# Kernel optimization log

Measured on AMD Instinct MI355X. Metric: run time of the kernel, lower is better.

The kernel has to match this reference:

```python
import jax, jax.numpy as jnp
import numpy as np

N_NODES = 50000
N_EDGES = 800000
N_RELS = 16
D = 128


def _rgcn_layer(h, W, b, loop_w, gate_w, src, dst, rel, norm, apply_relu, n_nodes):
    # Transform all node features by every relation weight once: [R, N, D_out].
    # Equivalent to DGL bmm_maybe_select's per-edge W[rel] bmm, but avoids an
    # [E, D, D] gather of weights.
    h_all = jnp.einsum('nd,rde->rne', h, W)
    msg = h_all[rel, src]                                    # [E, D_out]
    msg = msg * norm                                         # edge norm scaling
    gate_logit = jnp.einsum('nd,rd->rn', h, gate_w[..., 0])  # [R, N]
    gate = jax.nn.sigmoid(gate_logit[rel, src])[:, None]     # [E, 1]
    msg = msg * gate
    agg = jax.ops.segment_sum(msg, dst, num_segments=n_nodes)  # fn.sum -> dst
    out = agg + b + h @ loop_w                               # bias + self loop
    if apply_relu:
        out = jax.nn.relu(out)
    return out  # dropout is identity in eval mode


def setup_inputs() -> dict:
    key = jax.random.key(0)
    ks = jax.random.split(key, 12)
    gain = float(np.sqrt(2.0))  # relu gain (xavier-ish scale; values arbitrary)
    def xav(k, shape):
        fan = shape[-2] + shape[-1]
        s = gain * np.sqrt(6.0 / fan)
        return jax.random.uniform(k, shape, jnp.float32, -s, s)
    return {
        'h': jax.random.normal(ks[0], (N_NODES, D), jnp.float32),
        'norm': jax.random.uniform(ks[1], (N_EDGES, 1), jnp.float32),
        'weight0': xav(ks[2], (N_RELS, D, D)),
        'bias0': jnp.zeros((D,), jnp.float32),
        'loop_w0': xav(ks[3], (D, D)),
        'gate_w0': xav(ks[4], (N_RELS, D, 1)),
        'weight1': xav(ks[5], (N_RELS, D, D)),
        'bias1': jnp.zeros((D,), jnp.float32),
        'loop_w1': xav(ks[6], (D, D)),
        'gate_w1': xav(ks[7], (N_RELS, D, 1)),
        'src': jax.random.randint(ks[8], (N_EDGES,), 0, N_NODES, jnp.int32),
        'dst': jax.random.randint(ks[9], (N_EDGES,), 0, N_NODES, jnp.int32),
        'rel_type': jax.random.randint(ks[10], (N_EDGES,), 0, N_RELS, jnp.int32),
    }


def reference(h, norm, weight0, bias0, loop_w0, gate_w0,
              weight1, bias1, loop_w1, gate_w1, src, dst, rel_type):
    n_nodes = h.shape[0]
    # Layer 0: activation=relu (idx < num_hidden_layers - 1)
    h = _rgcn_layer(h, weight0, bias0, loop_w0, gate_w0, src, dst, rel_type,
                    norm, True, n_nodes)
    # Layer 1: no activation
    h = _rgcn_layer(h, weight1, bias1, loop_w1, gate_w1, src, dst, rel_type,
                    norm, False, n_nodes)
    return h
```

## Files before the change

### kernel.cpp

```cpp
#include <hip/hip_runtime.h>
#include <hip/hip_bf16.h>
#include <stdint.h>

#define NN 50000
#define NE 800000
#define NR 16
#define NP (NN * NR)
#define NB1 ((NP + 255) / 256)
#define NTILES ((NN + 127) / 128)

typedef unsigned short u16;
typedef unsigned int u32;

typedef __bf16 bf16x8 __attribute__((ext_vector_type(8)));
typedef __bf16 bf16x2 __attribute__((ext_vector_type(2)));
typedef float f32x4 __attribute__((ext_vector_type(4)));

__device__ __forceinline__ u16 f2bf(float f) {
  u32 u = __float_as_uint(f);
  u = u + 0x7FFFu + ((u >> 16) & 1u);
  return (u16)(u >> 16);
}

__device__ __forceinline__ u32 pk2bf(float x, float y) {
#if __has_builtin(__builtin_amdgcn_cvt_pk_bf16_f32)
  bf16x2 r = __builtin_amdgcn_cvt_pk_bf16_f32(x, y);
  union { bf16x2 v; u32 u; } c;
  c.v = r;
  return c.u;
#else
  return (u32)f2bf(x) | ((u32)f2bf(y) << 16);
#endif
}

__device__ __forceinline__ float bflo(u32 w) { return __uint_as_float(w << 16); }
__device__ __forceinline__ float bfhi(u32 w) { return __uint_as_float(w & 0xFFFF0000u); }

__global__ void hist_kernel(const int* __restrict__ dst, const int* __restrict__ rel,
                            int* __restrict__ counts) {
  int e = blockIdx.x * 256 + threadIdx.x;
  if (e < NE) atomicAdd(&counts[dst[e] * NR + rel[e]], 1);
}

__global__ void scan_partial(const int* __restrict__ counts, int* __restrict__ bsum) {
  __shared__ int buf[256];
  int t = threadIdx.x;
  int i = blockIdx.x * 256 + t;
  int v = (i < NP) ? counts[i] : 0;
  buf[t] = v;
  __syncthreads();
  for (int off = 1; off < 256; off <<= 1) {
    int x = buf[t];
    int y = (t >= off) ? buf[t - off] : 0;
    __syncthreads();
    buf[t] = x + y;
    __syncthreads();
  }
  if (t == 255) bsum[blockIdx.x] = buf[255];
}

__global__ void scan_mid(const int* __restrict__ bsum, int* __restrict__ boff,
                         int* __restrict__ total_out) {
  __shared__ int buf[1024];
  int t = threadIdx.x;
  int v[4];
  int sum = 0;
#pragma unroll
  for (int i = 0; i < 4; ++i) {
    int idx = t * 4 + i;
    v[i] = (idx < NB1) ? bsum[idx] : 0;
    sum += v[i];
  }
  buf[t] = sum;
  __syncthreads();
  for (int off = 1; off < 1024; off <<= 1) {
    int x = buf[t];
    int y = (t >= off) ? buf[t - off] : 0;
    __syncthreads();
    buf[t] = x + y;
    __syncthreads();
  }
  int excl = buf[t] - sum;
#pragma unroll
  for (int i = 0; i < 4; ++i) {
    int idx = t * 4 + i;
    if (idx < NB1) { boff[idx] = excl; excl += v[i]; }
  }
  if (t == 1023) *total_out = buf[1023];
}

__global__ void scan_final(const int* __restrict__ counts, const int* __restrict__ boff,
                           int* __restrict__ starts, int* __restrict__ cursor) {
  __shared__ int buf[256];
  int t = threadIdx.x;
  int i = blockIdx.x * 256 + t;
  int v = (i < NP) ? counts[i] : 0;
  buf[t] = v;
  __syncthreads();
  for (int off = 1; off < 256; off <<= 1) {
    int x = buf[t];
    int y = (t >= off) ? buf[t - off] : 0;
    __syncthreads();
    buf[t] = x + y;
    __syncthreads();
  }
  int s = boff[blockIdx.x] + buf[t] - v;
  if (i < NP) {
    starts[i] = s;
    cursor[i] = s;
  }
}

__global__ void scatter_kernel(const int* __restrict__ src, const int* __restrict__ dst,
                               const int* __restrict__ rel, const float* __restrict__ norm,
                               int* __restrict__ cursor, uint2* __restrict__ esd) {
  int e = blockIdx.x * 256 + threadIdx.x;
  if (e < NE) {
    int r = rel[e];
    int pos = atomicAdd(&cursor[dst[e] * NR + r], 1);
    esd[pos] = make_uint2(((u32)r << 16) | (u32)src[e], __float_as_uint(norm[e]));
  }
}

__global__ void convert_wt(const float* __restrict__ w0, const float* __restrict__ lw0,
                           const float* __restrict__ w1, const float* __restrict__ lw1,
                           u16* __restrict__ Wt) {
  int m = blockIdx.y;
  int idx = blockIdx.x * 256 + threadIdx.x;
  int d = idx >> 7, k = idx & 127;
  const float* s;
  if (m < 16) s = w0 + (size_t)m * 16384;
  else if (m == 16) s = lw0;
  else if (m < 33) s = w1 + (size_t)(m - 17) * 16384;
  else s = lw1;
  Wt[(size_t)m * 16384 + idx] = f2bf(s[k * 128 + d]);
}

__global__ void hconv_kernel(const float* __restrict__ h, u16* __restrict__ hbf) {
  int i = blockIdx.x * 256 + threadIdx.x;
  float4 v = ((const float4*)h)[i];
  ushort4 u;
  u.x = f2bf(v.x); u.y = f2bf(v.y); u.z = f2bf(v.z); u.w = f2bf(v.w);
  ((ushort4*)hbf)[i] = u;
}

__global__ void gates_kernel(const u16* __restrict__ hbf, const float* __restrict__ gw,
                             float* __restrict__ gates) {
  __shared__ float hs[16 * 132];
  __shared__ float gws[16 * 132];
  int t = threadIdx.x;
  int n0 = blockIdx.x * 16;
#pragma unroll
  for (int i = 0; i < 2; ++i) {
    int f = t + 256 * i;
    int row = f >> 5, c4 = (f & 31) * 4;
    ushort4 u = *(const ushort4*)&hbf[(size_t)(n0 + row) * 128 + c4];
    hs[row * 132 + c4 + 0] = __uint_as_float((u32)u.x << 16);
    hs[row * 132 + c4 + 1] = __uint_as_float((u32)u.y << 16);
    hs[row * 132 + c4 + 2] = __uint_as_float((u32)u.z << 16);
    hs[row * 132 + c4 + 3] = __uint_as_float((u32)u.w << 16);
    *(float4*)&gws[row * 132 + c4] = *(const float4*)&gw[row * 128 + c4];
  }
  __syncthreads();
  int nl = t >> 4, r = t & 15;
  float s = 0.f;
#pragma unroll 8
  for (int k = 0; k < 128; ++k) s += hs[nl * 132 + k] * gws[r * 132 + k];
  gates[r * NN + n0 + nl] = 1.f / (1.f + __expf(-s));
}

__global__ __launch_bounds__(256)
void aggregate_kernel(const u32* __restrict__ hbf32, const uint2* __restrict__ esd,
                      const float* __restrict__ gates, const int* __restrict__ starts,
                      u32* __restrict__ agg) {
  int wave = threadIdx.x >> 6, lane = threadIdx.x & 63;
  int v = blockIdx.x * 4 + wave;
  if (v >= NN) return;
  int s = starts[v * NR];
  int e = starts[v * NR + NR];
  u32* aggp = agg + (size_t)v * 64 + lane;
  float a0 = 0.f, a1 = 0.f;
  int cur = 0;
  int j = s;
  for (; j + 8 <= e; j += 8) {
    uint2 p[8];
#pragma unroll
    for (int i = 0; i < 8; ++i) p[i] = esd[j + i];
    u32 w[8];
    float gt[8];
#pragma unroll
    for (int i = 0; i < 8; ++i) {
      u32 rs = p[i].x;
      u32 sn = rs & 0xFFFFu;
      w[i] = hbf32[sn * 64u + (u32)lane];
      gt[i] = gates[(rs >> 16) * (u32)NN + sn];
    }
#pragma unroll
    for (int i = 0; i < 8; ++i) {
      int rel = (int)(p[i].x >> 16);
      while (cur < rel) {
        aggp[(size_t)cur * NN * 64] = pk2bf(a0, a1);
        a0 = 0.f; a1 = 0.f;
        ++cur;
      }
      float coef = gt[i] * __uint_as_float(p[i].y);
      a0 = fmaf(coef, bflo(w[i]), a0);
      a1 = fmaf(coef, bfhi(w[i]), a1);
    }
  }
  for (; j < e; ++j) {
    uint2 p = esd[j];
    u32 rs = p.x;
    u32 sn = rs & 0xFFFFu;
    int rel = (int)(rs >> 16);
    while (cur < rel) {
      aggp[(size_t)cur * NN * 64] = pk2bf(a0, a1);
      a0 = 0.f; a1 = 0.f;
      ++cur;
    }
    float coef = gates[(u32)rel * (u32)NN + sn] * __uint_as_float(p.y);
    u32 w = hbf32[sn * 64u + (u32)lane];
    a0 = fmaf(coef, bflo(w), a0);
    a1 = fmaf(coef, bfhi(w), a1);
  }
  while (cur < NR) {
    aggp[(size_t)cur * NN * 64] = pk2bf(a0, a1);
    a0 = 0.f; a1 = 0.f;
    ++cur;
  }
}


#define REP8(X) X(0) X(1) X(2) X(3) X(4) X(5) X(6) X(7)

#define BG_ISSUE(i)                                                           \
  {                                                                           \
    int u8 = t + 256 * i;                                                     \
    int row = u8 >> 4, c8 = (u8 & 15) * 8;                                    \
    int n = n0 + row;                                                         \
    int nc = n < NN ? n : NN - 1;                                             \
    rw##i = *(const uint4*)&wbase[row * 128 + c8];                            \
    ra##i = *(const uint4*)&srcbase[(size_t)nc * 128 + c8];                   \
  }

#define BG_COMMIT(i)                                                          \
  {                                                                           \
    int u8 = t + 256 * i;                                                     \
    int row = u8 >> 4, c8 = (u8 & 15) * 8;                                    \
    *(uint4*)&As[row * 136 + c8] = ra##i;                                     \
    *(uint4*)&Ws[row * 136 + c8] = rw##i;                                     \
  }

#define BG_MFMA                                                               \
  _Pragma("unroll")                                                           \
  for (int kk = 0; kk < 4; ++kk) {                                            \
    int k0 = kk * 32 + quad * 8;                                              \
    bf16x8 fa[4], fb[4];                                                      \
    _Pragma("unroll")                                                         \
    for (int i2 = 0; i2 < 4; ++i2)                                            \
      fa[i2] = *(const bf16x8*)&Ws[(wd + i2 * 16 + mrow) * 136 + k0];         \
    _Pragma("unroll")                                                         \
    for (int j2 = 0; j2 < 4; ++j2)                                            \
      fb[j2] = *(const bf16x8*)&As[(wn + j2 * 16 + mrow) * 136 + k0];         \
    _Pragma("unroll")                                                         \
    for (int i2 = 0; i2 < 4; ++i2)                                            \
      _Pragma("unroll")                                                       \
      for (int j2 = 0; j2 < 4; ++j2)                                          \
        acc[i2][j2] =                                                         \
            __builtin_amdgcn_mfma_f32_16x16x32_bf16(fa[i2], fb[j2],           \
                                                    acc[i2][j2], 0, 0, 0);    \
  }

template <int LAYER>
__global__ __launch_bounds__(256, 2)
void biggemm_kernel(const u16* __restrict__ aggu, const u16* __restrict__ hbf,
                    const u16* __restrict__ Wt, const float* __restrict__ bias,
                    u16* __restrict__ hb_out, float* __restrict__ fout) {
  __shared__ u16 As[128 * 136];
  __shared__ u16 Ws[128 * 136];
  int t = threadIdx.x;
  int n0 = blockIdx.x * 128;
  int wave = t >> 6, lane = t & 63;
  int wd = (wave & 1) * 64, wn = (wave >> 1) * 64;
  int mrow = lane & 15, quad = lane >> 4;
  float4 bv[4];
#pragma unroll
  for (int i = 0; i < 4; ++i) bv[i] = *(const float4*)&bias[wd + i * 16 + quad * 4];
  f32x4 acc[4][4];
#pragma unroll
  for (int i = 0; i < 4; ++i)
#pragma unroll
    for (int j = 0; j < 4; ++j) acc[i][j] = (f32x4){0.f, 0.f, 0.f, 0.f};

  uint4 ra0, ra1, ra2, ra3, ra4, ra5, ra6, ra7;
  uint4 rw0, rw1, rw2, rw3, rw4, rw5, rw6, rw7;
  const u16* srcbase = aggu;
  const u16* wbase = Wt;
  REP8(BG_ISSUE)
  for (int m = 0; m < 16; ++m) {
    REP8(BG_COMMIT)
    __syncthreads();
    int mm = m + 1;
    srcbase = (mm < 16) ? aggu + (size_t)mm * NN * 128 : hbf;
    wbase = Wt + (size_t)mm * 16384;
    REP8(BG_ISSUE)
    BG_MFMA
    __syncthreads();
  }
  REP8(BG_COMMIT)
  __syncthreads();
  BG_MFMA

#pragma unroll
  for (int j = 0; j < 4; ++j) {
    int n = n0 + wn + j * 16 + mrow;
    if (n < NN) {
#pragma unroll
      for (int i = 0; i < 4; ++i) {
        int d0 = wd + i * 16 + quad * 4;
        float v0 = acc[i][j][0] + bv[i].x;
        float v1 = acc[i][j][1] + bv[i].y;
        float v2 = acc[i][j][2] + bv[i].z;
        float v3 = acc[i][j][3] + bv[i].w;
        if (LAYER == 0) {
          v0 = fmaxf(v0, 0.f); v1 = fmaxf(v1, 0.f);
          v2 = fmaxf(v2, 0.f); v3 = fmaxf(v3, 0.f);
          uint2 st;
          st.x = pk2bf(v0, v1);
          st.y = pk2bf(v2, v3);
          *(uint2*)&hb_out[(size_t)n * 128 + d0] = st;
        } else {
          float4 st = make_float4(v0, v1, v2, v3);
          *(float4*)&fout[(size_t)n * 128 + d0] = st;
        }
      }
    }
  }
}

extern "C" void kernel_launch(void* const* d_in, const int* in_sizes, int n_in,
                              void* d_out, int out_size, void* d_ws, size_t ws_size,
                              hipStream_t stream) {
  const float* h0   = (const float*)d_in[0];
  const float* norm = (const float*)d_in[1];
  const float* w0   = (const float*)d_in[2];
  const float* b0   = (const float*)d_in[3];
  const float* lw0  = (const float*)d_in[4];
  const float* gw0  = (const float*)d_in[5];
  const float* w1   = (const float*)d_in[6];
  const float* b1   = (const float*)d_in[7];
  const float* lw1  = (const float*)d_in[8];
  const float* gw1  = (const float*)d_in[9];
  const int*   src  = (const int*)d_in[10];
  const int*   dst  = (const int*)d_in[11];
  const int*   rel  = (const int*)d_in[12];
  float* out = (float*)d_out;

  char* p = (char*)d_ws;
  auto alloc = [&](size_t bytes) -> void* {
    void* q = (void*)p;
    p += (bytes + 255) & ~(size_t)255;
    return q;
  };
  u16*   Wt     = (u16*)alloc((size_t)34 * 16384 * 2);
  float* gates  = (float*)alloc((size_t)NR * NN * 4);
  u16*   hbf0   = (u16*)alloc((size_t)NN * 128 * 2);
  u16*   hbf1   = (u16*)alloc((size_t)NN * 128 * 2);
  int*   counts = (int*)alloc((size_t)NP * 4);
  int*   cursor = (int*)alloc((size_t)NP * 4);
  int*   starts = (int*)alloc((size_t)(NP + 1) * 4);
  int*   bsum   = (int*)alloc((size_t)NB1 * 4);
  int*   boff   = (int*)alloc((size_t)NB1 * 4);
  uint2* esd    = (uint2*)alloc((size_t)NE * 8);
  u32*   agg    = (u32*)alloc((size_t)NN * NR * 64 * 4);

  hipMemsetAsync(counts, 0, (size_t)NP * 4, stream);
  hist_kernel<<<NE / 256, 256, 0, stream>>>(dst, rel, counts);
  scan_partial<<<NB1, 256, 0, stream>>>(counts, bsum);
  scan_mid<<<1, 1024, 0, stream>>>(bsum, boff, starts + NP);
  scan_final<<<NB1, 256, 0, stream>>>(counts, boff, starts, cursor);
  scatter_kernel<<<NE / 256, 256, 0, stream>>>(src, dst, rel, norm, cursor, esd);
  convert_wt<<<dim3(64, 34), 256, 0, stream>>>(w0, lw0, w1, lw1, Wt);
  hconv_kernel<<<NN * 32 / 256, 256, 0, stream>>>(h0, hbf0);

  gates_kernel<<<NN / 16, 256, 0, stream>>>(hbf0, gw0, gates);
  aggregate_kernel<<<(NN + 3) / 4, 256, 0, stream>>>(
      (const u32*)hbf0, esd, gates, starts, agg);
  biggemm_kernel<0><<<NTILES, 256, 0, stream>>>(
      (const u16*)agg, hbf0, Wt, b0, hbf1, nullptr);

  gates_kernel<<<NN / 16, 256, 0, stream>>>(hbf1, gw1, gates);
  aggregate_kernel<<<(NN + 3) / 4, 256, 0, stream>>>(
      (const u32*)hbf1, esd, gates, starts, agg);
  biggemm_kernel<1><<<NTILES, 256, 0, stream>>>(
      (const u16*)agg, hbf1, Wt + (size_t)17 * 16384, b1, nullptr, out);
}
```

Measured before the change: 451.8 us.

## Fuse edge aggregation into GEMM with relation-major edge ordering

Re-sorts edges by (relation, destination) and fuses message aggregation into the relation GEMM, so each block aggregates its 128-node tile per relation directly into shared memory before the MFMA step. This eliminates the large intermediate per-relation aggregate buffer write and reread. Weight fragments are now loaded from global into registers instead of shared memory. The cost is far fewer waves doing the latency-bound gathers, plus higher register pressure.

```diff
diff --git a/kernel.cpp b/kernel.cpp
--- a/kernel.cpp
+++ b/kernel.cpp
@@ -39,7 +39,7 @@
 __global__ void hist_kernel(const int* __restrict__ dst, const int* __restrict__ rel,
                             int* __restrict__ counts) {
   int e = blockIdx.x * 256 + threadIdx.x;
-  if (e < NE) atomicAdd(&counts[dst[e] * NR + rel[e]], 1);
+  if (e < NE) atomicAdd(&counts[rel[e] * NN + dst[e]], 1);
 }
 
 __global__ void scan_partial(const int* __restrict__ counts, int* __restrict__ bsum) {
@@ -116,9 +116,9 @@
                                int* __restrict__ cursor, uint2* __restrict__ esd) {
   int e = blockIdx.x * 256 + threadIdx.x;
   if (e < NE) {
-    int r = rel[e];
-    int pos = atomicAdd(&cursor[dst[e] * NR + r], 1);
-    esd[pos] = make_uint2(((u32)r << 16) | (u32)src[e], __float_as_uint(norm[e]));
+    int d = dst[e];
+    int pos = atomicAdd(&cursor[rel[e] * NN + d], 1);
+    esd[pos] = make_uint2(((u32)d << 16) | (u32)src[e], __float_as_uint(norm[e]));
   }
 }
 
@@ -169,147 +169,127 @@
   gates[r * NN + n0 + nl] = 1.f / (1.f + __expf(-s));
 }
 
-__global__ __launch_bounds__(256)
-void aggregate_kernel(const u32* __restrict__ hbf32, const uint2* __restrict__ esd,
-                      const float* __restrict__ gates, const int* __restrict__ starts,
-                      u32* __restrict__ agg) {
-  int wave = threadIdx.x >> 6, lane = threadIdx.x & 63;
-  int v = blockIdx.x * 4 + wave;
-  if (v >= NN) return;
-  int s = starts[v * NR];
-  int e = starts[v * NR + NR];
-  u32* aggp = agg + (size_t)v * 64 + lane;
-  float a0 = 0.f, a1 = 0.f;
-  int cur = 0;
-  int j = s;
-  for (; j + 8 <= e; j += 8) {
-    uint2 p[8];
-#pragma unroll
-    for (int i = 0; i < 8; ++i) p[i] = esd[j + i];
-    u32 w[8];
-    float gt[8];
-#pragma unroll
-    for (int i = 0; i < 8; ++i) {
-      u32 rs = p[i].x;
-      u32 sn = rs & 0xFFFFu;
-      w[i] = hbf32[sn * 64u + (u32)lane];
-      gt[i] = gates[(rs >> 16) * (u32)NN + sn];
-    }
-#pragma unroll
-    for (int i = 0; i < 8; ++i) {
-      int rel = (int)(p[i].x >> 16);
-      while (cur < rel) {
-        aggp[(size_t)cur * NN * 64] = pk2bf(a0, a1);
-        a0 = 0.f; a1 = 0.f;
-        ++cur;
-      }
-      float coef = gt[i] * __uint_as_float(p[i].y);
-      a0 = fmaf(coef, bflo(w[i]), a0);
-      a1 = fmaf(coef, bfhi(w[i]), a1);
-    }
-  }
-  for (; j < e; ++j) {
-    uint2 p = esd[j];
-    u32 rs = p.x;
-    u32 sn = rs & 0xFFFFu;
-    int rel = (int)(rs >> 16);
-    while (cur < rel) {
-      aggp[(size_t)cur * NN * 64] = pk2bf(a0, a1);
-      a0 = 0.f; a1 = 0.f;
-      ++cur;
-    }
-    float coef = gates[(u32)rel * (u32)NN + sn] * __uint_as_float(p.y);
-    u32 w = hbf32[sn * 64u + (u32)lane];
-    a0 = fmaf(coef, bflo(w), a0);
-    a1 = fmaf(coef, bfhi(w), a1);
-  }
-  while (cur < NR) {
-    aggp[(size_t)cur * NN * 64] = pk2bf(a0, a1);
-    a0 = 0.f; a1 = 0.f;
-    ++cur;
-  }
-}
-
-
-#define REP8(X) X(0) X(1) X(2) X(3) X(4) X(5) X(6) X(7)
-
-#define BG_ISSUE(i)                                                           \
-  {                                                                           \
-    int u8 = t + 256 * i;                                                     \
-    int row = u8 >> 4, c8 = (u8 & 15) * 8;                                    \
-    int n = n0 + row;                                                         \
-    int nc = n < NN ? n : NN - 1;                                             \
-    rw##i = *(const uint4*)&wbase[row * 128 + c8];                            \
-    ra##i = *(const uint4*)&srcbase[(size_t)nc * 128 + c8];                   \
-  }
-
-#define BG_COMMIT(i)                                                          \
-  {                                                                           \
-    int u8 = t + 256 * i;                                                     \
-    int row = u8 >> 4, c8 = (u8 & 15) * 8;                                    \
-    *(uint4*)&As[row * 136 + c8] = ra##i;                                     \
-    *(uint4*)&Ws[row * 136 + c8] = rw##i;                                     \
-  }
-
-#define BG_MFMA                                                               \
-  _Pragma("unroll")                                                           \
-  for (int kk = 0; kk < 4; ++kk) {                                            \
-    int k0 = kk * 32 + quad * 8;                                              \
-    bf16x8 fa[4], fb[4];                                                      \
-    _Pragma("unroll")                                                         \
-    for (int i2 = 0; i2 < 4; ++i2)                                            \
-      fa[i2] = *(const bf16x8*)&Ws[(wd + i2 * 16 + mrow) * 136 + k0];         \
-    _Pragma("unroll")                                                         \
-    for (int j2 = 0; j2 < 4; ++j2)                                            \
-      fb[j2] = *(const bf16x8*)&As[(wn + j2 * 16 + mrow) * 136 + k0];         \
-    _Pragma("unroll")                                                         \
-    for (int i2 = 0; i2 < 4; ++i2)                                            \
-      _Pragma("unroll")                                                       \
-      for (int j2 = 0; j2 < 4; ++j2)                                          \
-        acc[i2][j2] =                                                         \
-            __builtin_amdgcn_mfma_f32_16x16x32_bf16(fa[i2], fb[j2],           \
-                                                    acc[i2][j2], 0, 0, 0);    \
-  }
-
 template <int LAYER>
 __global__ __launch_bounds__(256, 2)
-void biggemm_kernel(const u16* __restrict__ aggu, const u16* __restrict__ hbf,
-                    const u16* __restrict__ Wt, const float* __restrict__ bias,
-                    u16* __restrict__ hb_out, float* __restrict__ fout) {
+void fused_kernel(const u16* __restrict__ hbf, const uint2* __restrict__ esd,
+                  const float* __restrict__ gates, const int* __restrict__ starts,
+                  const u16* __restrict__ Wt, const float* __restrict__ bias,
+                  u16* __restrict__ hb_out, float* __restrict__ fout) {
   __shared__ u16 As[128 * 136];
-  __shared__ u16 Ws[128 * 136];
+  const u32* hbf32 = (const u32*)hbf;
   int t = threadIdx.x;
   int n0 = blockIdx.x * 128;
   int wave = t >> 6, lane = t & 63;
   int wd = (wave & 1) * 64, wn = (wave >> 1) * 64;
   int mrow = lane & 15, quad = lane >> 4;
+  int vbase = n0 + wave * 32;
+
   float4 bv[4];
 #pragma unroll
   for (int i = 0; i < 4; ++i) bv[i] = *(const float4*)&bias[wd + i * 16 + quad * 4];
+
   f32x4 acc[4][4];
 #pragma unroll
   for (int i = 0; i < 4; ++i)
 #pragma unroll
     for (int j = 0; j < 4; ++j) acc[i][j] = (f32x4){0.f, 0.f, 0.f, 0.f};
 
-  uint4 ra0, ra1, ra2, ra3, ra4, ra5, ra6, ra7;
-  uint4 rw0, rw1, rw2, rw3, rw4, rw5, rw6, rw7;
-  const u16* srcbase = aggu;
-  const u16* wbase = Wt;
-  REP8(BG_ISSUE)
-  for (int m = 0; m < 16; ++m) {
-    REP8(BG_COMMIT)
-    __syncthreads();
-    int mm = m + 1;
-    srcbase = (mm < 16) ? aggu + (size_t)mm * NN * 128 : hbf;
-    wbase = Wt + (size_t)mm * 16384;
-    REP8(BG_ISSUE)
-    BG_MFMA
-    __syncthreads();
-  }
-  REP8(BG_COMMIT)
-  __syncthreads();
-  BG_MFMA
+  u32* asp = (u32*)As + (wave * 32) * 68 + lane;
+
+  for (int m = 0; m < 17; ++m) {
+    bf16x8 fw[4][4];
+    {
+      const u16* wmat = Wt + (size_t)m * 16384;
+#pragma unroll
+      for (int kk = 0; kk < 4; ++kk)
+#pragma unroll
+        for (int i2 = 0; i2 < 4; ++i2)
+          fw[kk][i2] = *(const bf16x8*)&wmat[(wd + i2 * 16 + mrow) * 128 + kk * 32 + quad * 8];
+    }
+
+    if (m < 16) {
+      float a0 = 0.f, a1 = 0.f;
+      int cur = 0;
+      int s = 0, e = 0;
+      if (vbase < NN) {
+        int vend = vbase + 32;
+        if (vend > NN) vend = NN;
+        s = starts[m * NN + vbase];
+        e = starts[m * NN + vend];
+      }
+      int j = s;
+      for (; j + 8 <= e; j += 8) {
+        uint2 p[8];
+#pragma unroll
+        for (int i = 0; i < 8; ++i) p[i] = esd[j + i];
+        u32 w[8];
+        float gt[8];
+#pragma unroll
+        for (int i = 0; i < 8; ++i) {
+          u32 sn = p[i].x & 0xFFFFu;
+          w[i] = hbf32[sn * 64u + (u32)lane];
+          gt[i] = gates[(u32)m * (u32)NN + sn];
+        }
+#pragma unroll
+        for (int i = 0; i < 8; ++i) {
+          int local = (int)(p[i].x >> 16) - vbase;
+          while (cur < local) {
+            asp[cur * 68] = pk2bf(a0, a1);
+            a0 = 0.f; a1 = 0.f;
+            ++cur;
+          }
+          float coef = gt[i] * __uint_as_float(p[i].y);
+          a0 = fmaf(coef, bflo(w[i]), a0);
+          a1 = fmaf(coef, bfhi(w[i]), a1);
+        }
+      }
+      for (; j < e; ++j) {
+        uint2 p = esd[j];
+        u32 sn = p.x & 0xFFFFu;
+        int local = (int)(p.x >> 16) - vbase;
+        while (cur < local) {
+          asp[cur * 68] = pk2bf(a0, a1);
+          a0 = 0.f; a1 = 0.f;
+          ++cur;
+        }
+        float coef = gates[(u32)m * (u32)NN + sn] * __uint_as_float(p.y);
+        u32 w = hbf32[sn * 64u + (u32)lane];
+        a0 = fmaf(coef, bflo(w), a0);
+        a1 = fmaf(coef, bfhi(w), a1);
+      }
+      while (cur < 32) {
+        asp[cur * 68] = pk2bf(a0, a1);
+        a0 = 0.f; a1 = 0.f;
+        ++cur;
+      }
+    } else {
+#pragma unroll
+      for (int i = 0; i < 8; ++i) {
+        int u8 = t + 256 * i;
+        int row = u8 >> 4, c8 = (u8 & 15) * 8;
+        int n = n0 + row;
+        int nc = n < NN ? n : NN - 1;
+        *(uint4*)&As[row * 136 + c8] = *(const uint4*)&hbf[(size_t)nc * 128 + c8];
+      }
+    }
+    __syncthreads();
+
+#pragma unroll
+    for (int kk = 0; kk < 4; ++kk) {
+      int k0 = kk * 32 + quad * 8;
+      bf16x8 fb[4];
+#pragma unroll
+      for (int j2 = 0; j2 < 4; ++j2)
+        fb[j2] = *(const bf16x8*)&As[(wn + j2 * 16 + mrow) * 136 + k0];
+#pragma unroll
+      for (int i2 = 0; i2 < 4; ++i2)
+#pragma unroll
+        for (int j2 = 0; j2 < 4; ++j2)
+          acc[i2][j2] = __builtin_amdgcn_mfma_f32_16x16x32_bf16(fw[kk][i2], fb[j2],
+                                                                acc[i2][j2], 0, 0, 0);
+    }
+    __syncthreads();
+  }
 
 #pragma unroll
   for (int j = 0; j < 4; ++j) {
@@ -372,7 +352,6 @@
   int*   bsum   = (int*)alloc((size_t)NB1 * 4);
   int*   boff   = (int*)alloc((size_t)NB1 * 4);
   uint2* esd    = (uint2*)alloc((size_t)NE * 8);
-  u32*   agg    = (u32*)alloc((size_t)NN * NR * 64 * 4);
 
   hipMemsetAsync(counts, 0, (size_t)NP * 4, stream);
   hist_kernel<<<NE / 256, 256, 0, stream>>>(dst, rel, counts);
@@ -384,14 +363,11 @@
   hconv_kernel<<<NN * 32 / 256, 256, 0, stream>>>(h0, hbf0);
 
   gates_kernel<<<NN / 16, 256, 0, stream>>>(hbf0, gw0, gates);
-  aggregate_kernel<<<(NN + 3) / 4, 256, 0, stream>>>(
-      (const u32*)hbf0, esd, gates, starts, agg);
-  biggemm_kernel<0><<<NTILES, 256, 0, stream>>>(
-      (const u16*)agg, hbf0, Wt, b0, hbf1, nullptr);
+  fused_kernel<0><<<NTILES, 256, 0, stream>>>(hbf0, esd, gates, starts, Wt, b0,
+                                              hbf1, nullptr);
 
   gates_kernel<<<NN / 16, 256, 0, stream>>>(hbf1, gw1, gates);
-  aggregate_kernel<<<(NN + 3) / 4, 256, 0, stream>>>(
-      (const u32*)hbf1, esd, gates, starts, agg);
-  biggemm_kernel<1><<<NTILES, 256, 0, stream>>>(
-      (const u16*)agg, hbf1, Wt + (size_t)17 * 16384, b1, nullptr, out);
-}
+  fused_kernel<1><<<NTILES, 256, 0, stream>>>(hbf1, esd, gates, starts,
+                                              Wt + (size_t)17 * 16384, b1,
+                                              nullptr, out);
+}
```

Result: slower. 623.4 us (+38.0%).
